# Optimization experiments

Measured on AMD Instinct MI355X. Metric: run time of the kernel, lower is better.

Reference implementation:

```python
import jax, jax.numpy as jnp
import numpy as np
from jax import lax

CONTEXT = 7
EPS = 1e-5  # BatchNorm2d default eps
DN = ('NCHW', 'OIHW', 'NCHW')


def _cbr(x, W, b, g, be, m, v, padding):
    # conv2d + BatchNorm (eval, running stats) + ReLU
    y = lax.conv_general_dilated(x, W, (1, 1), padding, dimension_numbers=DN)
    y = y + b[None, :, None, None]
    y = (y - m[None, :, None, None]) * (g / jnp.sqrt(v + EPS))[None, :, None, None] + be[None, :, None, None]
    return jax.nn.relu(y)


def _pool21(x):  # MaxPool2d(kernel_size=(2,1))
    return lax.reduce_window(x, -jnp.inf, lax.max, (1, 1, 2, 1), (1, 1, 2, 1), 'VALID')


def setup_inputs() -> dict:
    key = jax.random.key(0)
    ks = jax.random.split(key, 16)
    B, T, F, NC = 16, 108, 144, 25
    d = {}
    d['x'] = jax.random.normal(ks[0], (B, T, F), jnp.float32)
    d['labels'] = jax.random.randint(ks[1], (B, T), 0, NC)
    shapes = [(32, 1, 3, 3), (32, 32, 3, 3), (32, 32, 3, 3), (32, 32, 3, 3),
              (64, 32, 3, 3), (64, 64, 3, 3), (128, 64, 12, 9)]
    for i, s in enumerate(shapes, 1):
        fan_in = s[1] * s[2] * s[3]
        d[f'W{i}'] = jax.random.normal(ks[1 + i], s, jnp.float32) / np.sqrt(fan_in).astype(np.float32)
        c = s[0]
        d[f'b{i}'] = jnp.zeros((c,), jnp.float32)
        d[f'g{i}'] = jnp.ones((c,), jnp.float32)
        d[f'be{i}'] = jnp.zeros((c,), jnp.float32)
        d[f'm{i}'] = jnp.zeros((c,), jnp.float32)
        d[f'v{i}'] = jnp.ones((c,), jnp.float32)
    d['W8'] = jax.random.normal(ks[9], (NC, 128, 1, 1), jnp.float32) / np.float32(np.sqrt(128.0))
    d['b8'] = jnp.zeros((NC,), jnp.float32)
    return d


def reference(x, labels,
              W1, b1, g1, be1, m1, v1,
              W2, b2, g2, be2, m2, v2,
              W3, b3, g3, be3, m3, v3,
              W4, b4, g4, be4, m4, v4,
              W5, b5, g5, be5, m5, v5,
              W6, b6, g6, be6, m6, v6,
              W7, b7, g7, be7, m7, v7,
              W8, b8):
    B, T, F = x.shape
    win_len = 2 * CONTEXT + 1
    # permute to [B, F, T], zero-pad time by CONTEXT on both sides
    xp = jnp.pad(jnp.transpose(x, (0, 2, 1)), ((0, 0), (0, 0), (CONTEXT, CONTEXT)))
    # vectorized sliding windows (replaces the nested python loop of slices+cat)
    idx = jnp.arange(T)[:, None] + jnp.arange(win_len)[None, :]  # [T, 15]
    win = xp[:, :, idx]                                          # [B, F, T, 15]
    h = jnp.transpose(win, (0, 2, 1, 3)).reshape(B * T, 1, F, win_len)
    h = _cbr(h, W1, b1, g1, be1, m1, v1, 'SAME')
    h = _cbr(h, W2, b2, g2, be2, m2, v2, 'SAME')
    h = _cbr(h, W3, b3, g3, be3, m3, v3, 'SAME')
    h = _cbr(h, W4, b4, g4, be4, m4, v4, 'SAME')
    h = _pool21(h)  # dropout2d is identity in eval
    h = _cbr(h, W5, b5, g5, be5, m5, v5, 'VALID')
    h = _cbr(h, W6, b6, g6, be6, m6, v6, 'VALID')
    h = _pool21(h)
    h = _cbr(h, W7, b7, g7, be7, m7, v7, 'VALID')
    h = lax.conv_general_dilated(h, W8, (1, 1), 'VALID', dimension_numbers=DN) + b8[None, :, None, None]
    logits = jnp.mean(h, axis=(2, 3))  # AvgPool2d over full spatial extent
    return logits.reshape(B, T, -1)    # probs_out=True -> CRF input
```

## Files before the change

### kernel.cpp

```cpp
#include <hip/hip_runtime.h>
#include <hip/hip_bf16.h>
#include <hip/hip_fp16.h>

#define TA 71680
#define SLOT 108544
#define C6N 23936

typedef _Float16 v8h __attribute__((ext_vector_type(8)));
typedef float v4f __attribute__((ext_vector_type(4)));
typedef unsigned short u16x8 __attribute__((ext_vector_type(8)));

__device__ inline float h2f(unsigned short u) {
    union { unsigned short s; _Float16 h; } v; v.s = u; return (float)v.h;
}
__device__ inline unsigned short f2h(float f) {
    union { unsigned short s; _Float16 h; } v; v.h = (_Float16)f; return v.s;
}

__global__ void repack_k(const float* __restrict__ W, const float* __restrict__ bb,
                         const float* __restrict__ gg, const float* __restrict__ be,
                         const float* __restrict__ mm, const float* __restrict__ vv,
                         float* __restrict__ wOut, float* __restrict__ tOut,
                         int CIN, int KHW, int COUT)
{
    int gid = blockIdx.x * 256 + threadIdx.x;
    if (gid < COUT) {
        float s = gg[gid] * rsqrtf(vv[gid] + 1e-5f);
        tOut[gid] = (bb[gid] - mm[gid]) * s + be[gid];
    }
    int tot = CIN * KHW * COUT;
    if (gid >= tot) return;
    int co = gid % COUT;
    int rest = gid / COUT;
    int k = rest % KHW;
    int ci = rest / KHW;
    float s = gg[co] * rsqrtf(vv[co] + 1e-5f);
    wOut[gid] = W[(co * CIN + ci) * KHW + k] * s;
}

__global__ void repack_mfma_k(const float* __restrict__ W, const float* __restrict__ bb,
                              const float* __restrict__ gg, const float* __restrict__ be,
                              const float* __restrict__ mm, const float* __restrict__ vv,
                              unsigned short* __restrict__ frag, float* __restrict__ tOut,
                              int CIN, int NT, int HALVES)
{
    int gid = blockIdx.x * 256 + threadIdx.x;
    int COUT = NT * 16;
    if (gid < COUT) {
        float s = gg[gid] * rsqrtf(vv[gid] + 1e-5f);
        tOut[gid] = (bb[gid] - mm[gid]) * s + be[gid];
    }
    int tot = 9 * HALVES * NT * 512;
    if (gid >= tot) return;
    int j    = gid & 7;
    int lane = (gid >> 3) & 63;
    int nt   = (gid >> 9) % NT;
    int rest = (gid >> 9) / NT;
    int half = rest % HALVES;
    int khw  = rest / HALVES;
    int ci   = half * 32 + (lane >> 4) * 8 + j;
    int co   = nt * 16 + (lane & 15);
    int kh   = khw / 3, kw = khw % 3;
    float s = gg[co] * rsqrtf(vv[co] + 1e-5f);
    frag[gid] = f2h(W[((co * CIN + ci) * 3 + kh) * 3 + kw] * s);
}

__global__ void repack7_k(const float* __restrict__ W, const float* __restrict__ bb,
                          const float* __restrict__ gg, const float* __restrict__ be,
                          const float* __restrict__ mm, const float* __restrict__ vv,
                          unsigned short* __restrict__ frag, float* __restrict__ tOut)
{
    int gid = blockIdx.x * 256 + threadIdx.x;
    if (gid < 128) {
        float s = gg[gid] * rsqrtf(vv[gid] + 1e-5f);
        tOut[gid] = (bb[gid] - mm[gid]) * s + be[gid];
    }
    if (gid >= 884736) return;
    int j    = gid & 7;
    int lane = (gid >> 3) & 63;
    int nt   = (gid >> 9) & 7;
    int half = (gid >> 12) & 1;
    int khw  = gid >> 13;
    int co   = nt * 16 + (lane & 15);
    int ci   = half * 32 + (lane >> 4) * 8 + j;
    int kh   = khw / 9, kw = khw - kh * 9;
    float s = gg[co] * rsqrtf(vv[co] + 1e-5f);
    frag[gid] = f2h(W[((co * 64 + ci) * 12 + kh) * 9 + kw] * s);
}

__global__ __launch_bounds__(256) void conv1234f_k(
    const float* __restrict__ x, unsigned short* __restrict__ out,
    const float* __restrict__ wr1, const float* __restrict__ t1v,
    const unsigned short* __restrict__ f2, const unsigned short* __restrict__ f3,
    const unsigned short* __restrict__ f4, const float* __restrict__ t2,
    const float* __restrict__ t3, const float* __restrict__ t4, int c0)
{
    __shared__ __align__(16) unsigned short sm[23728];
    float* sx = (float*)(sm + 22912);
    const int band = blockIdx.x;
    const int nl = blockIdx.y;
    const int n = c0 + nl;
    const int tid = threadIdx.x;
    const int wave = tid >> 6, lane = tid & 63;
    const int m = lane & 15, quad = lane >> 4;
    const int b = n / 108, t = n - b * 108;

    {
        float4* dst = (float4*)sm;
        for (int i = tid; i < 568; i += 256) {
            if (i < 408) {
                int tp = i / 24, fp = i - tp * 24;
                int tt = t - 8 + tp;
                int ff = band * 16 - 4 + fp;
                float v = 0.f;
                if (tt >= 0 && tt < 108 && ff >= 0 && ff < 144)
                    v = x[(b * 108 + tt) * 144 + ff];
                sx[tp * 24 + fp] = v;
            } else {
                int j = i - 408;
                int q = j / 40, jj = j - q * 40;
                int rr = jj >> 1, c2 = (jj & 1) * 16;
                dst[1500 + q * 341 + rr * 17 + c2] = (float4){0.f,0.f,0.f,0.f};
            }
        }
    }
    __syncthreads();

    for (int e = tid; e < 374; e += 256) {
        int r = e / 17, cp = e - r * 17;
        int gr = band * 16 - 3 + r;
        int gc = cp - 1;
        float acc1[32];
#pragma unroll
        for (int i = 0; i < 32; ++i) acc1[i] = 0.f;
        bool valid = (gr >= 0 && gr < 144 && gc >= 0 && gc < 15);
        if (valid) {
#pragma unroll
            for (int kh = 0; kh < 3; ++kh) {
                int fp = r + kh;
#pragma unroll
                for (int kw = 0; kw < 3; ++kw) {
                    int c = gc + kw - 1;
                    if (c < 0 || c >= 15) continue;
                    float xv = sx[(c + 1) * 24 + fp];
                    const float* wp = wr1 + (kh * 3 + kw) * 32;
#pragma unroll
                    for (int q8 = 0; q8 < 8; ++q8) {
                        float4 wv = *(const float4*)(wp + q8 * 4);
                        acc1[q8 * 4 + 0] = fmaf(xv, wv.x, acc1[q8 * 4 + 0]);
                        acc1[q8 * 4 + 1] = fmaf(xv, wv.y, acc1[q8 * 4 + 1]);
                        acc1[q8 * 4 + 2] = fmaf(xv, wv.z, acc1[q8 * 4 + 2]);
                        acc1[q8 * 4 + 3] = fmaf(xv, wv.w, acc1[q8 * 4 + 3]);
                    }
                }
            }
        }
#pragma unroll
        for (int q2 = 0; q2 < 4; ++q2) {
            u16x8 pk;
#pragma unroll
            for (int c8 = 0; c8 < 8; ++c8)
                pk[c8] = valid ? f2h(fmaxf(acc1[q2 * 8 + c8] + t1v[q2 * 8 + c8], 0.f))
                               : (unsigned short)0;
            *(u16x8*)(sm + q2 * 3000 + (r * 17 + cp) * 8) = pk;
        }
    }
    __syncthreads();

    v4f acc[2][5];
    int mt[5], la[5];

#pragma unroll
    for (int wt = 0; wt < 5; ++wt) {
        int tt = wave * 5 + wt; if (tt > 18) tt = 18;
        mt[wt] = tt;
        int p = tt * 16 + m; if (p >= 300) p = 299;
        int r = p / 15, c = p - r * 15;
        la[wt] = r * 17 + c;
    }
#pragma unroll
    for (int nt = 0; nt < 2; ++nt)
#pragma unroll
        for (int wt = 0; wt < 5; ++wt) acc[nt][wt] = (v4f){0.f,0.f,0.f,0.f};
#pragma unroll
    for (int khw = 0; khw < 9; ++khw) {
        const int sh = (khw / 3) * 17 + (khw % 3);
        v8h a[5];
#pragma unroll
        for (int wt = 0; wt < 5; ++wt)
            a[wt] = *(const v8h*)(sm + quad * 3000 + (la[wt] + sh) * 8);
#pragma unroll
        for (int nt = 0; nt < 2; ++nt) {
            v8h bb = *(const v8h*)(f2 + (khw * 2 + nt) * 512 + lane * 8);
#pragma unroll
            for (int wt = 0; wt < 5; ++wt)
                acc[nt][wt] = __builtin_amdgcn_mfma_f32_16x16x32_f16(a[wt], bb, acc[nt][wt], 0, 0, 0);
        }
    }
#pragma unroll
    for (int wt = 0; wt < 5; ++wt) {
        const int pb = mt[wt] * 16 + quad * 4;
#pragma unroll
        for (int nt = 0; nt < 2; ++nt) {
            const int co = nt * 16 + m;
            const float tb = t2[co];
            unsigned short* ob = sm + 12000 + (co >> 3) * 2728 + (co & 7);
#pragma unroll
            for (int reg = 0; reg < 4; ++reg) {
                int p = pb + reg;
                if (p < 300) {
                    int r = p / 15, c = p - r * 15;
                    ob[(r * 17 + c + 1) * 8] = f2h(fmaxf(acc[nt][wt][reg] + tb, 0.f));
                }
            }
        }
    }
    __syncthreads();

    if (tid < 144) {
        int q = tid / 36, jj = tid - q * 36;
        int rr = jj >> 1, c2 = (jj & 1) * 16;
        *(float4*)((float4*)sm + q * 307 + rr * 17 + c2) = (float4){0.f,0.f,0.f,0.f};
    }

#pragma unroll
    for (int wt = 0; wt < 5; ++wt) {
        int tt = wave * 5 + wt; if (tt > 16) tt = 16;
        mt[wt] = tt;
        int p = tt * 16 + m; if (p >= 270) p = 269;
        int r = p / 15, c = p - r * 15;
        la[wt] = r * 17 + c;
    }
#pragma unroll
    for (int nt = 0; nt < 2; ++nt)
#pragma unroll
        for (int wt = 0; wt < 5; ++wt) acc[nt][wt] = (v4f){0.f,0.f,0.f,0.f};
#pragma unroll
    for (int khw = 0; khw < 9; ++khw) {
        const int sh = (khw / 3) * 17 + (khw % 3);
        v8h a[5];
#pragma unroll
        for (int wt = 0; wt < 5; ++wt)
            a[wt] = *(const v8h*)(sm + 12000 + quad * 2728 + (la[wt] + sh) * 8);
#pragma unroll
        for (int nt = 0; nt < 2; ++nt) {
            v8h bb = *(const v8h*)(f3 + (khw * 2 + nt) * 512 + lane * 8);
#pragma unroll
            for (int wt = 0; wt < 5; ++wt)
                acc[nt][wt] = __builtin_amdgcn_mfma_f32_16x16x32_f16(a[wt], bb, acc[nt][wt], 0, 0, 0);
        }
    }
#pragma unroll
    for (int wt = 0; wt < 5; ++wt) {
        const int pb = mt[wt] * 16 + quad * 4;
#pragma unroll
        for (int nt = 0; nt < 2; ++nt) {
            const int co = nt * 16 + m;
            const float tb = t3[co];
            unsigned short* ob = sm + (co >> 3) * 2456 + (co & 7);
#pragma unroll
            for (int reg = 0; reg < 4; ++reg) {
                int p = pb + reg;
                if (p < 270) {
                    int r = p / 15, c = p - r * 15;
                    ob[(r * 17 + c + 1) * 8] = f2h(fmaxf(acc[nt][wt][reg] + tb, 0.f));
                }
            }
        }
    }
    __syncthreads();

    int mt4[4], la4[4];
#pragma unroll
    for (int wt = 0; wt < 4; ++wt) {
        int tt = wave * 4 + wt; if (tt > 14) tt = 14;
        mt4[wt] = tt;
        int p = tt * 16 + m;
        int pr = p / 30, rem = p - pr * 30;
        int w = rem >> 1, r4 = pr * 2 + (rem & 1);
        la4[wt] = r4 * 17 + w;
    }
    v4f acc4[2][4];
#pragma unroll
    for (int nt = 0; nt < 2; ++nt)
#pragma unroll
        for (int wt = 0; wt < 4; ++wt) acc4[nt][wt] = (v4f){0.f,0.f,0.f,0.f};
#pragma unroll
    for (int khw = 0; khw < 9; ++khw) {
        const int sh = (khw / 3) * 17 + (khw % 3);
        v8h a[4];
#pragma unroll
        for (int wt = 0; wt < 4; ++wt)
            a[wt] = *(const v8h*)(sm + quad * 2456 + (la4[wt] + sh) * 8);
#pragma unroll
        for (int nt = 0; nt < 2; ++nt) {
            v8h bb = *(const v8h*)(f4 + (khw * 2 + nt) * 512 + lane * 8);
#pragma unroll
            for (int wt = 0; wt < 4; ++wt)
                acc4[nt][wt] = __builtin_amdgcn_mfma_f32_16x16x32_f16(a[wt], bb, acc4[nt][wt], 0, 0, 0);
        }
    }
    unsigned short* outN = out + (size_t)nl * SLOT;
#pragma unroll
    for (int wt = 0; wt < 4; ++wt) {
        const int pb = band * 240 + mt4[wt] * 16 + quad * 4;
#pragma unroll
        for (int nt = 0; nt < 2; ++nt) {
            const int co = nt * 16 + m;
            const float tb = t4[co];
            unsigned short* ob = outN + (co >> 3) * 9216 + (co & 7);
#pragma unroll
            for (int pi = 0; pi < 2; ++pi) {
                int pe = pb + pi * 2;
                int pr = pe / 30, rem = pe - pr * 30, w = rem >> 1;
                float v0 = fmaxf(acc4[nt][wt][pi * 2] + tb, 0.f);
                float v1 = fmaxf(acc4[nt][wt][pi * 2 + 1] + tb, 0.f);
                ob[(pr * 16 + w) * 8] = f2h(fmaxf(v0, v1));
            }
        }
    }
}

__global__ __launch_bounds__(256) void conv5m_k(
    const unsigned short* __restrict__ in, unsigned short* __restrict__ out,
    const unsigned short* __restrict__ frag, const float* __restrict__ tv)
{
    const int n = blockIdx.y;
    const int tid = threadIdx.x;
    const int wave = tid >> 6, lane = tid & 63;
    const int m = lane & 15, quad = lane >> 4;
    const unsigned short* inN = in + (size_t)n * SLOT + quad * 9216;

    int mt[2], a0[2];
#pragma unroll
    for (int wt = 0; wt < 2; ++wt) {
        int t = blockIdx.x * 8 + wave * 2 + wt; if (t > 56) t = 56;
        mt[wt] = t;
        int p = t * 16 + m; if (p > 909) p = 909;
        int r = p / 13, w = p - r * 13;
        a0[wt] = (r * 16 + w) * 8;
    }

    v4f acc[4][2];
#pragma unroll
    for (int nt = 0; nt < 4; ++nt)
#pragma unroll
        for (int wt = 0; wt < 2; ++wt) acc[nt][wt] = (v4f){0.f,0.f,0.f,0.f};

#pragma unroll
    for (int khw = 0; khw < 9; ++khw) {
        const int shift = ((khw / 3) * 16 + (khw % 3)) * 8;
        v8h a[2];
#pragma unroll
        for (int wt = 0; wt < 2; ++wt)
            a[wt] = *(const v8h*)(inN + a0[wt] + shift);
#pragma unroll
        for (int nt = 0; nt < 4; ++nt) {
            v8h b = *(const v8h*)(frag + (khw * 4 + nt) * 512 + lane * 8);
#pragma unroll
            for (int wt = 0; wt < 2; ++wt)
                acc[nt][wt] = __builtin_amdgcn_mfma_f32_16x16x32_f16(a[wt], b, acc[nt][wt], 0, 0, 0);
        }
    }

    unsigned short* outN = out + (size_t)n * SLOT;
#pragma unroll
    for (int wt = 0; wt < 2; ++wt) {
        const int pb = mt[wt] * 16 + quad * 4;
#pragma unroll
        for (int nt = 0; nt < 4; ++nt) {
            const int co = nt * 16 + m;
            const float tb = tv[co];
            unsigned short* ob = outN + (co >> 3) * 8960 + (co & 7);
#pragma unroll
            for (int reg = 0; reg < 4; ++reg) {
                int p = pb + reg;
                if (p < 910) {
                    int r = p / 13, w = p - r * 13;
                    ob[(r * 16 + w) * 8] = f2h(fmaxf(acc[nt][wt][reg] + tb, 0.f));
                }
            }
        }
    }
}

__global__ __launch_bounds__(256) void conv6m_k(
    const unsigned short* __restrict__ in, unsigned short* __restrict__ c6,
    const unsigned short* __restrict__ frag, const float* __restrict__ tv)
{
    const int n = blockIdx.y;
    const int tid = threadIdx.x;
    const int wave = tid >> 6, lane = tid & 63;
    const int m = lane & 15, quad = lane >> 4;
    const unsigned short* inN = in + (size_t)n * SLOT;

    int mt[2], a0[2];
#pragma unroll
    for (int wt = 0; wt < 2; ++wt) {
        int t = blockIdx.x * 8 + wave * 2 + wt; if (t > 46) t = 46;
        mt[wt] = t;
        int p = t * 16 + m; if (p > 747) p = 747;
        int pr = p / 22, rem = p - pr * 22;
        int w = rem >> 1, r = pr * 2 + (rem & 1);
        a0[wt] = (r * 16 + w) * 8;
    }

    v4f acc[4][2];
#pragma unroll
    for (int nt = 0; nt < 4; ++nt)
#pragma unroll
        for (int wt = 0; wt < 2; ++wt) acc[nt][wt] = (v4f){0.f,0.f,0.f,0.f};

#pragma unroll
    for (int khw = 0; khw < 9; ++khw) {
        const int shift = ((khw / 3) * 16 + (khw % 3)) * 8;
#pragma unroll
        for (int half = 0; half < 2; ++half) {
            const unsigned short* ip = inN + (half * 4 + quad) * 8960 + shift;
            v8h a[2];
#pragma unroll
            for (int wt = 0; wt < 2; ++wt)
                a[wt] = *(const v8h*)(ip + a0[wt]);
#pragma unroll
            for (int nt = 0; nt < 4; ++nt) {
                v8h b = *(const v8h*)(frag + ((khw * 2 + half) * 4 + nt) * 512 + lane * 8);
#pragma unroll
                for (int wt = 0; wt < 2; ++wt)
                    acc[nt][wt] = __builtin_amdgcn_mfma_f32_16x16x32_f16(a[wt], b, acc[nt][wt], 0, 0, 0);
            }
        }
    }

    unsigned short* outN = c6 + (size_t)n * C6N;
#pragma unroll
    for (int wt = 0; wt < 2; ++wt) {
        const int pb = mt[wt] * 16 + quad * 4;
#pragma unroll
        for (int nt = 0; nt < 4; ++nt) {
            const int co = nt * 16 + m;
            const float tb = tv[co];
            unsigned short* ob = outN + (co >> 3) * 2992 + (co & 7);
#pragma unroll
            for (int pi = 0; pi < 2; ++pi) {
                int pe = pb + pi * 2;
                if (pe < 748) {
                    int pr = pe / 22, rem = pe - pr * 22, w = rem >> 1;
                    float v0 = fmaxf(acc[nt][wt][pi * 2] + tb, 0.f);
                    float v1 = fmaxf(acc[nt][wt][pi * 2 + 1] + tb, 0.f);
                    ob[(pr * 11 + w) * 8] = f2h(fmaxf(v0, v1));
                }
            }
        }
    }
}

__global__ __launch_bounds__(256) void conv7mfma_k(
    const unsigned short* __restrict__ c6, float* __restrict__ pooled,
    const unsigned short* __restrict__ frag7, const float* __restrict__ tv)
{
    __shared__ __align__(16) unsigned short sA[14176];
    const int n = blockIdx.x;
    const int tid = threadIdx.x;
    const int wave = tid >> 6;
    const int lane = tid & 63;
    const int m = lane & 15;
    const int quad = lane >> 4;

    int pm[5];
#pragma unroll
    for (int mt = 0; mt < 5; ++mt) {
        int p = mt * 16 + m;
        if (p >= 69) p = 0;
        pm[mt] = (p / 3) * 13 + (p % 3);
    }

    v4f acc[2][5];
#pragma unroll
    for (int t = 0; t < 2; ++t)
#pragma unroll
        for (int mt = 0; mt < 5; ++mt)
            acc[t][mt] = (v4f){0.f, 0.f, 0.f, 0.f};

    for (int half = 0; half < 2; ++half) {
        __syncthreads();
        {
            const float4* src = (const float4*)(c6 + (size_t)n * C6N + half * 11968);
            float4* dst = (float4*)sA;
            for (int i = tid; i < 1496; i += 256) {
                int q = i / 374, pos = i - q * 374;
                int h = pos / 11, w = pos - h * 11;
                dst[q * 443 + h * 13 + w] = src[i];
            }
        }
        __syncthreads();
        for (int khw = 0; khw < 108; ++khw) {
            const int off = (khw / 9) * 13 + (khw % 9);
            v8h a[5];
#pragma unroll
            for (int mt = 0; mt < 5; ++mt)
                a[mt] = *(const v8h*)(sA + (quad * 443 + pm[mt] + off) * 8);
            const unsigned short* bp = frag7
                + ((size_t)(khw * 2 + half) * 8) * 512 + lane * 8;
#pragma unroll
            for (int t = 0; t < 2; ++t) {
                const int nt = wave + t * 4;
                v8h b = *(const v8h*)(bp + nt * 512);
#pragma unroll
                for (int mt = 0; mt < 5; ++mt)
                    acc[t][mt] = __builtin_amdgcn_mfma_f32_16x16x32_f16(
                        a[mt], b, acc[t][mt], 0, 0, 0);
            }
        }
    }

    float s[2] = {0.f, 0.f};
#pragma unroll
    for (int t = 0; t < 2; ++t) {
        const float tb = tv[(wave + t * 4) * 16 + m];
#pragma unroll
        for (int mt = 0; mt < 5; ++mt) {
#pragma unroll
            for (int rr = 0; rr < 4; ++rr) {
                int p = mt * 16 + quad * 4 + rr;
                if (p < 69) s[t] += fmaxf(acc[t][mt][rr] + tb, 0.f);
            }
        }
    }
#pragma unroll
    for (int t = 0; t < 2; ++t) {
        s[t] += __shfl_xor(s[t], 16);
        s[t] += __shfl_xor(s[t], 32);
    }
    if (lane < 16) {
#pragma unroll
        for (int t = 0; t < 2; ++t)
            pooled[(size_t)n * 128 + (wave + t * 4) * 16 + lane] = s[t] * (1.f / 69.f);
    }
}

__global__ void logits_k(const float* __restrict__ pooled, const float* __restrict__ W8,
                         const float* __restrict__ b8, float* __restrict__ outg,
                         int total)
{
    int gid = blockIdx.x * 256 + threadIdx.x;
    if (gid >= total * 25) return;
    int nl = gid / 25, c = gid - nl * 25;
    const float* pp = pooled + (size_t)nl * 128;
    const float* wp = W8 + c * 128;
    float s = b8[c];
#pragma unroll
    for (int ci = 0; ci < 128; ci += 4) {
        float4 wv = *(const float4*)(wp + ci);
        float4 pv = *(const float4*)(pp + ci);
        s = fmaf(wv.x, pv.x, s);
        s = fmaf(wv.y, pv.y, s);
        s = fmaf(wv.z, pv.z, s);
        s = fmaf(wv.w, pv.w, s);
    }
    outg[(size_t)nl * 25 + c] = s;
}

extern "C" void kernel_launch(void* const* d_in, const int* in_sizes, int n_in,
                              void* d_out, int out_size, void* d_ws, size_t ws_size,
                              hipStream_t stream)
{
    const float* x = (const float*)d_in[0];
    const float* Wl[8]; const float* bl[8]; const float* gl[8];
    const float* bel[8]; const float* ml[8]; const float* vl[8];
    for (int i = 1; i <= 7; ++i) {
        int o = 2 + (i - 1) * 6;
        Wl[i]  = (const float*)d_in[o + 0];
        bl[i]  = (const float*)d_in[o + 1];
        gl[i]  = (const float*)d_in[o + 2];
        bel[i] = (const float*)d_in[o + 3];
        ml[i]  = (const float*)d_in[o + 4];
        vl[i]  = (const float*)d_in[o + 5];
    }
    const float* W8 = (const float*)d_in[44];
    const float* b8 = (const float*)d_in[45];
    float* ws = (float*)d_ws;

    float* wr1 = ws + 0;        float* t1 = ws + 288;
    unsigned short* f2b = (unsigned short*)(ws + 320);
    float* t2 = ws + 4928;
    unsigned short* f3b = (unsigned short*)(ws + 4960);
    float* t3 = ws + 9568;
    unsigned short* f4b = (unsigned short*)(ws + 9600);
    float* t4 = ws + 14208;
    unsigned short* f5b = (unsigned short*)(ws + 14240);
    float* t5 = ws + 23456;
    unsigned short* f6b = (unsigned short*)(ws + 23520);
    float* t6 = ws + 41952;
    unsigned short* f7b = (unsigned short*)(ws + 42016);
    float* t7 = ws + 484384;
    const size_t WFL = 484512;

    unsigned short* c6buf = (unsigned short*)(ws + WFL);
    const size_t C6FL = (size_t)1728 * C6N / 2;
    float* pooled = ws + WFL + C6FL;
    const size_t FIXED = WFL + C6FL + (size_t)1728 * 128;

    size_t avail_fl = ws_size / 4;
    size_t buf_halves = (avail_fl > FIXED) ? (avail_fl - FIXED) * 2 : 0;
    int Cs = (int)(buf_halves / (size_t)SLOT);
    if (Cs < 1) Cs = 1;
    if (Cs > 1728) Cs = 1728;
    unsigned short* bufA = (unsigned short*)(ws + FIXED);
    unsigned short* bufB = bufA + TA;

    auto g1 = [](int t) { return (t + 255) / 256; };

    repack_k<<<g1(288), 256, 0, stream>>>(Wl[1], bl[1], gl[1], bel[1], ml[1], vl[1], wr1, t1, 1, 9, 32);
    repack_mfma_k<<<g1(9216),  256, 0, stream>>>(Wl[2], bl[2], gl[2], bel[2], ml[2], vl[2], f2b, t2, 32, 2, 1);
    repack_mfma_k<<<g1(9216),  256, 0, stream>>>(Wl[3], bl[3], gl[3], bel[3], ml[3], vl[3], f3b, t3, 32, 2, 1);
    repack_mfma_k<<<g1(9216),  256, 0, stream>>>(Wl[4], bl[4], gl[4], bel[4], ml[4], vl[4], f4b, t4, 32, 2, 1);
    repack_mfma_k<<<g1(18432), 256, 0, stream>>>(Wl[5], bl[5], gl[5], bel[5], ml[5], vl[5], f5b, t5, 32, 4, 1);
    repack_mfma_k<<<g1(36864), 256, 0, stream>>>(Wl[6], bl[6], gl[6], bel[6], ml[6], vl[6], f6b, t6, 64, 4, 2);
    repack7_k<<<g1(884736), 256, 0, stream>>>(Wl[7], bl[7], gl[7], bel[7], ml[7], vl[7], f7b, t7);

    for (int c0 = 0; c0 < 1728; c0 += Cs) {
        int cn = (1728 - c0 < Cs) ? (1728 - c0) : Cs;
        conv1234f_k<<<dim3(9, cn), 256, 0, stream>>>(x, bufB, wr1, t1,
                                                     f2b, f3b, f4b, t2, t3, t4, c0);
        conv5m_k<<<dim3(8, cn), 256, 0, stream>>>(bufB, bufA, f5b, t5);
        conv6m_k<<<dim3(6, cn), 256, 0, stream>>>(bufA, c6buf + (size_t)c0 * C6N, f6b, t6);
    }

    conv7mfma_k<<<1728, 256, 0, stream>>>(c6buf, pooled, f7b, t7);
    logits_k<<<g1(1728 * 25), 256, 0, stream>>>(pooled, W8, b8, (float*)d_out, 1728);
}
```

Before: 1.130 ms.

## Shrink conv1-4 fused band to 12 rows and split conv1 channels across threads

The fused conv1-4 kernel now processes 12 output frequency rows per block instead of 16, giving 12 bands per sample instead of 9. Shared memory per block and per-wave MFMA tiles shrink, which should allow more resident blocks per CU and better load balance. The conv1 scalar stage is split so each thread computes 8 of the 32 channels at one position, cutting its register footprint and spreading the work over more threads. In exchange the halo rows (3 on each side) are recomputed more often relative to useful output.

```diff
diff --git a/kernel.cpp b/kernel.cpp
--- a/kernel.cpp
+++ b/kernel.cpp
@@ -95,8 +95,8 @@
     const unsigned short* __restrict__ f4, const float* __restrict__ t2,
     const float* __restrict__ t3, const float* __restrict__ t4, int c0)
 {
-    __shared__ __align__(16) unsigned short sm[23728];
-    float* sx = (float*)(sm + 22912);
+    __shared__ __align__(16) unsigned short sm[19240];
+    float* sx = (float*)(sm + 18560);
     const int band = blockIdx.x;
     const int nl = blockIdx.y;
     const int n = c0 + nl;
@@ -107,33 +107,33 @@
 
     {
         float4* dst = (float4*)sm;
-        for (int i = tid; i < 568; i += 256) {
-            if (i < 408) {
-                int tp = i / 24, fp = i - tp * 24;
+        for (int i = tid; i < 468; i += 256) {
+            if (i < 340) {
+                int tp = i / 20, fp = i - tp * 20;
                 int tt = t - 8 + tp;
-                int ff = band * 16 - 4 + fp;
+                int ff = band * 12 - 4 + fp;
                 float v = 0.f;
                 if (tt >= 0 && tt < 108 && ff >= 0 && ff < 144)
                     v = x[(b * 108 + tt) * 144 + ff];
-                sx[tp * 24 + fp] = v;
+                sx[tp * 20 + fp] = v;
             } else {
-                int j = i - 408;
-                int q = j / 40, jj = j - q * 40;
+                int j = i - 340;
+                int q = j >> 5, jj = j & 31;
                 int rr = jj >> 1, c2 = (jj & 1) * 16;
-                dst[1500 + q * 341 + rr * 17 + c2] = (float4){0.f,0.f,0.f,0.f};
+                dst[1228 + q * 273 + rr * 17 + c2] = (float4){0.f,0.f,0.f,0.f};
             }
         }
     }
     __syncthreads();
 
-    for (int e = tid; e < 374; e += 256) {
-        int r = e / 17, cp = e - r * 17;
-        int gr = band * 16 - 3 + r;
-        int gc = cp - 1;
-        float acc1[32];
-#pragma unroll
-        for (int i = 0; i < 32; ++i) acc1[i] = 0.f;
+    for (int e = tid; e < 1224; e += 256) {
+        int pos = e >> 2, qg = e & 3;
+        int r = pos / 17, cp = pos - r * 17;
+        int gr = band * 12 - 3 + r, gc = cp - 1;
         bool valid = (gr >= 0 && gr < 144 && gc >= 0 && gc < 15);
+        float acc1[8];
+#pragma unroll
+        for (int i = 0; i < 8; ++i) acc1[i] = 0.f;
         if (valid) {
 #pragma unroll
             for (int kh = 0; kh < 3; ++kh) {
@@ -142,73 +142,123 @@
                 for (int kw = 0; kw < 3; ++kw) {
                     int c = gc + kw - 1;
                     if (c < 0 || c >= 15) continue;
-                    float xv = sx[(c + 1) * 24 + fp];
-                    const float* wp = wr1 + (kh * 3 + kw) * 32;
-#pragma unroll
-                    for (int q8 = 0; q8 < 8; ++q8) {
-                        float4 wv = *(const float4*)(wp + q8 * 4);
-                        acc1[q8 * 4 + 0] = fmaf(xv, wv.x, acc1[q8 * 4 + 0]);
-                        acc1[q8 * 4 + 1] = fmaf(xv, wv.y, acc1[q8 * 4 + 1]);
-                        acc1[q8 * 4 + 2] = fmaf(xv, wv.z, acc1[q8 * 4 + 2]);
-                        acc1[q8 * 4 + 3] = fmaf(xv, wv.w, acc1[q8 * 4 + 3]);
-                    }
+                    float xv = sx[(c + 1) * 20 + fp];
+                    const float* wp = wr1 + (kh * 3 + kw) * 32 + qg * 8;
+                    float4 wA = *(const float4*)(wp);
+                    float4 wB = *(const float4*)(wp + 4);
+                    acc1[0] = fmaf(xv, wA.x, acc1[0]);
+                    acc1[1] = fmaf(xv, wA.y, acc1[1]);
+                    acc1[2] = fmaf(xv, wA.z, acc1[2]);
+                    acc1[3] = fmaf(xv, wA.w, acc1[3]);
+                    acc1[4] = fmaf(xv, wB.x, acc1[4]);
+                    acc1[5] = fmaf(xv, wB.y, acc1[5]);
+                    acc1[6] = fmaf(xv, wB.z, acc1[6]);
+                    acc1[7] = fmaf(xv, wB.w, acc1[7]);
                 }
             }
         }
-#pragma unroll
-        for (int q2 = 0; q2 < 4; ++q2) {
-            u16x8 pk;
-#pragma unroll
-            for (int c8 = 0; c8 < 8; ++c8)
-                pk[c8] = valid ? f2h(fmaxf(acc1[q2 * 8 + c8] + t1v[q2 * 8 + c8], 0.f))
-                               : (unsigned short)0;
-            *(u16x8*)(sm + q2 * 3000 + (r * 17 + cp) * 8) = pk;
-        }
+        u16x8 pk;
+#pragma unroll
+        for (int c8 = 0; c8 < 8; ++c8)
+            pk[c8] = valid ? f2h(fmaxf(acc1[c8] + t1v[qg * 8 + c8], 0.f))
+                           : (unsigned short)0;
+        *(u16x8*)(sm + qg * 2456 + pos * 8) = pk;
     }
     __syncthreads();
 
-    v4f acc[2][5];
-    int mt[5], la[5];
-
-#pragma unroll
-    for (int wt = 0; wt < 5; ++wt) {
-        int tt = wave * 5 + wt; if (tt > 18) tt = 18;
+    v4f acc[2][4];
+    int mt[4], la[4];
+
+#pragma unroll
+    for (int wt = 0; wt < 4; ++wt) {
+        int tt = wave * 4 + wt; if (tt > 14) tt = 14;
         mt[wt] = tt;
-        int p = tt * 16 + m; if (p >= 300) p = 299;
+        int p = tt * 16 + m;
         int r = p / 15, c = p - r * 15;
         la[wt] = r * 17 + c;
     }
 #pragma unroll
     for (int nt = 0; nt < 2; ++nt)
 #pragma unroll
-        for (int wt = 0; wt < 5; ++wt) acc[nt][wt] = (v4f){0.f,0.f,0.f,0.f};
+        for (int wt = 0; wt < 4; ++wt) acc[nt][wt] = (v4f){0.f,0.f,0.f,0.f};
 #pragma unroll
     for (int khw = 0; khw < 9; ++khw) {
         const int sh = (khw / 3) * 17 + (khw % 3);
-        v8h a[5];
-#pragma unroll
-        for (int wt = 0; wt < 5; ++wt)
-            a[wt] = *(const v8h*)(sm + quad * 3000 + (la[wt] + sh) * 8);
+        v8h a[4];
+#pragma unroll
+        for (int wt = 0; wt < 4; ++wt)
+            a[wt] = *(const v8h*)(sm + quad * 2456 + (la[wt] + sh) * 8);
 #pragma unroll
         for (int nt = 0; nt < 2; ++nt) {
             v8h bb = *(const v8h*)(f2 + (khw * 2 + nt) * 512 + lane * 8);
 #pragma unroll
-            for (int wt = 0; wt < 5; ++wt)
+            for (int wt = 0; wt < 4; ++wt)
                 acc[nt][wt] = __builtin_amdgcn_mfma_f32_16x16x32_f16(a[wt], bb, acc[nt][wt], 0, 0, 0);
         }
     }
 #pragma unroll
-    for (int wt = 0; wt < 5; ++wt) {
+    for (int wt = 0; wt < 4; ++wt) {
         const int pb = mt[wt] * 16 + quad * 4;
 #pragma unroll
         for (int nt = 0; nt < 2; ++nt) {
             const int co = nt * 16 + m;
             const float tb = t2[co];
-            unsigned short* ob = sm + 12000 + (co >> 3) * 2728 + (co & 7);
+            unsigned short* ob = sm + 9824 + (co >> 3) * 2184 + (co & 7);
 #pragma unroll
             for (int reg = 0; reg < 4; ++reg) {
                 int p = pb + reg;
-                if (p < 300) {
+                int r = p / 15, c = p - r * 15;
+                ob[(r * 17 + c + 1) * 8] = f2h(fmaxf(acc[nt][wt][reg] + tb, 0.f));
+            }
+        }
+    }
+    __syncthreads();
+
+    if (tid < 112) {
+        int q = tid / 28, jj = tid - q * 28;
+        int rr = jj >> 1, c2 = (jj & 1) * 16;
+        *((float4*)sm + q * 239 + rr * 17 + c2) = (float4){0.f,0.f,0.f,0.f};
+    }
+
+#pragma unroll
+    for (int wt = 0; wt < 4; ++wt) {
+        int tt = wave * 4 + wt; if (tt > 13) tt = 13;
+        mt[wt] = tt;
+        int p = tt * 16 + m; if (p >= 210) p = 209;
+        int r = p / 15, c = p - r * 15;
+        la[wt] = r * 17 + c;
+    }
+#pragma unroll
+    for (int nt = 0; nt < 2; ++nt)
+#pragma unroll
+        for (int wt = 0; wt < 4; ++wt) acc[nt][wt] = (v4f){0.f,0.f,0.f,0.f};
+#pragma unroll
+    for (int khw = 0; khw < 9; ++khw) {
+        const int sh = (khw / 3) * 17 + (khw % 3);
+        v8h a[4];
+#pragma unroll
+        for (int wt = 0; wt < 4; ++wt)
+            a[wt] = *(const v8h*)(sm + 9824 + quad * 2184 + (la[wt] + sh) * 8);
+#pragma unroll
+        for (int nt = 0; nt < 2; ++nt) {
+            v8h bb = *(const v8h*)(f3 + (khw * 2 + nt) * 512 + lane * 8);
+#pragma unroll
+            for (int wt = 0; wt < 4; ++wt)
+                acc[nt][wt] = __builtin_amdgcn_mfma_f32_16x16x32_f16(a[wt], bb, acc[nt][wt], 0, 0, 0);
+        }
+    }
+#pragma unroll
+    for (int wt = 0; wt < 4; ++wt) {
+        const int pb = mt[wt] * 16 + quad * 4;
+#pragma unroll
+        for (int nt = 0; nt < 2; ++nt) {
+            const int co = nt * 16 + m;
+            const float tb = t3[co];
+            unsigned short* ob = sm + (co >> 3) * 1912 + (co & 7);
+#pragma unroll
+            for (int reg = 0; reg < 4; ++reg) {
+                int p = pb + reg;
+                if (p < 210) {
                     int r = p / 15, c = p - r * 15;
                     ob[(r * 17 + c + 1) * 8] = f2h(fmaxf(acc[nt][wt][reg] + tb, 0.f));
                 }
@@ -217,93 +267,41 @@
     }
     __syncthreads();
 
-    if (tid < 144) {
-        int q = tid / 36, jj = tid - q * 36;
-        int rr = jj >> 1, c2 = (jj & 1) * 16;
-        *(float4*)((float4*)sm + q * 307 + rr * 17 + c2) = (float4){0.f,0.f,0.f,0.f};
-    }
-
-#pragma unroll
-    for (int wt = 0; wt < 5; ++wt) {
-        int tt = wave * 5 + wt; if (tt > 16) tt = 16;
-        mt[wt] = tt;
-        int p = tt * 16 + m; if (p >= 270) p = 269;
-        int r = p / 15, c = p - r * 15;
-        la[wt] = r * 17 + c;
-    }
-#pragma unroll
-    for (int nt = 0; nt < 2; ++nt)
-#pragma unroll
-        for (int wt = 0; wt < 5; ++wt) acc[nt][wt] = (v4f){0.f,0.f,0.f,0.f};
-#pragma unroll
-    for (int khw = 0; khw < 9; ++khw) {
-        const int sh = (khw / 3) * 17 + (khw % 3);
-        v8h a[5];
-#pragma unroll
-        for (int wt = 0; wt < 5; ++wt)
-            a[wt] = *(const v8h*)(sm + 12000 + quad * 2728 + (la[wt] + sh) * 8);
-#pragma unroll
-        for (int nt = 0; nt < 2; ++nt) {
-            v8h bb = *(const v8h*)(f3 + (khw * 2 + nt) * 512 + lane * 8);
-#pragma unroll
-            for (int wt = 0; wt < 5; ++wt)
-                acc[nt][wt] = __builtin_amdgcn_mfma_f32_16x16x32_f16(a[wt], bb, acc[nt][wt], 0, 0, 0);
-        }
-    }
-#pragma unroll
-    for (int wt = 0; wt < 5; ++wt) {
-        const int pb = mt[wt] * 16 + quad * 4;
-#pragma unroll
-        for (int nt = 0; nt < 2; ++nt) {
-            const int co = nt * 16 + m;
-            const float tb = t3[co];
-            unsigned short* ob = sm + (co >> 3) * 2456 + (co & 7);
-#pragma unroll
-            for (int reg = 0; reg < 4; ++reg) {
-                int p = pb + reg;
-                if (p < 270) {
-                    int r = p / 15, c = p - r * 15;
-                    ob[(r * 17 + c + 1) * 8] = f2h(fmaxf(acc[nt][wt][reg] + tb, 0.f));
-                }
-            }
-        }
-    }
-    __syncthreads();
-
-    int mt4[4], la4[4];
-#pragma unroll
-    for (int wt = 0; wt < 4; ++wt) {
-        int tt = wave * 4 + wt; if (tt > 14) tt = 14;
+    int mt4[3], la4[3];
+#pragma unroll
+    for (int wt = 0; wt < 3; ++wt) {
+        int tt = wave * 3 + wt;
         mt4[wt] = tt;
-        int p = tt * 16 + m;
+        int p = tt * 16 + m; if (p >= 180) p = 179;
         int pr = p / 30, rem = p - pr * 30;
         int w = rem >> 1, r4 = pr * 2 + (rem & 1);
         la4[wt] = r4 * 17 + w;
     }
-    v4f acc4[2][4];
+    v4f acc4[2][3];
 #pragma unroll
     for (int nt = 0; nt < 2; ++nt)
 #pragma unroll
-        for (int wt = 0; wt < 4; ++wt) acc4[nt][wt] = (v4f){0.f,0.f,0.f,0.f};
+        for (int wt = 0; wt < 3; ++wt) acc4[nt][wt] = (v4f){0.f,0.f,0.f,0.f};
 #pragma unroll
     for (int khw = 0; khw < 9; ++khw) {
         const int sh = (khw / 3) * 17 + (khw % 3);
-        v8h a[4];
-#pragma unroll
-        for (int wt = 0; wt < 4; ++wt)
-            a[wt] = *(const v8h*)(sm + quad * 2456 + (la4[wt] + sh) * 8);
+        v8h a[3];
+#pragma unroll
+        for (int wt = 0; wt < 3; ++wt)
+            a[wt] = *(const v8h*)(sm + quad * 1912 + (la4[wt] + sh) * 8);
 #pragma unroll
         for (int nt = 0; nt < 2; ++nt) {
             v8h bb = *(const v8h*)(f4 + (khw * 2 + nt) * 512 + lane * 8);
 #pragma unroll
-            for (int wt = 0; wt < 4; ++wt)
+            for (int wt = 0; wt < 3; ++wt)
                 acc4[nt][wt] = __builtin_amdgcn_mfma_f32_16x16x32_f16(a[wt], bb, acc4[nt][wt], 0, 0, 0);
         }
     }
     unsigned short* outN = out + (size_t)nl * SLOT;
 #pragma unroll
-    for (int wt = 0; wt < 4; ++wt) {
-        const int pb = band * 240 + mt4[wt] * 16 + quad * 4;
+    for (int wt = 0; wt < 3; ++wt) {
+        const int pl = mt4[wt] * 16 + quad * 4;
+        const int pb = band * 180 + pl;
 #pragma unroll
         for (int nt = 0; nt < 2; ++nt) {
             const int co = nt * 16 + m;
@@ -311,11 +309,13 @@
             unsigned short* ob = outN + (co >> 3) * 9216 + (co & 7);
 #pragma unroll
             for (int pi = 0; pi < 2; ++pi) {
-                int pe = pb + pi * 2;
-                int pr = pe / 30, rem = pe - pr * 30, w = rem >> 1;
-                float v0 = fmaxf(acc4[nt][wt][pi * 2] + tb, 0.f);
-                float v1 = fmaxf(acc4[nt][wt][pi * 2 + 1] + tb, 0.f);
-                ob[(pr * 16 + w) * 8] = f2h(fmaxf(v0, v1));
+                if (pl + pi * 2 < 180) {
+                    int pe = pb + pi * 2;
+                    int pr = pe / 30, rem = pe - pr * 30, w = rem >> 1;
+                    float v0 = fmaxf(acc4[nt][wt][pi * 2] + tb, 0.f);
+                    float v1 = fmaxf(acc4[nt][wt][pi * 2 + 1] + tb, 0.f);
+                    ob[(pr * 16 + w) * 8] = f2h(fmaxf(v0, v1));
+                }
             }
         }
     }
@@ -620,8 +620,8 @@
 
     for (int c0 = 0; c0 < 1728; c0 += Cs) {
         int cn = (1728 - c0 < Cs) ? (1728 - c0) : Cs;
-        conv1234f_k<<<dim3(9, cn), 256, 0, stream>>>(x, bufB, wr1, t1,
-                                                     f2b, f3b, f4b, t2, t3, t4, c0);
+        conv1234f_k<<<dim3(12, cn), 256, 0, stream>>>(x, bufB, wr1, t1,
+                                                      f2b, f3b, f4b, t2, t3, t4, c0);
         conv5m_k<<<dim3(8, cn), 256, 0, stream>>>(bufB, bufA, f5b, t5);
         conv6m_k<<<dim3(6, cn), 256, 0, stream>>>(bufA, c6buf + (size_t)c0 * C6N, f6b, t6);
     }
```

After: 1.313 ms. 16.2% more time.
